# Kernel tuning notes

Hardware: AMD Instinct MI355X
Metric: run time of the kernel (lower is better)

Reference implementation:

```python
import jax, jax.numpy as jnp
import numpy as np

N_NODES = 50000
N_EDGES = 400000
D_IN = 128
D_H = 128
N_CLASSES = 20
N_GRAPHS = 256
EPS_BN = 1e-5


def _lin_params(key, d_in, d_out, scale=0.05):
    kw, kb = jax.random.split(key)
    W = jax.random.normal(kw, (d_in, d_out), jnp.float32) * scale
    b = jax.random.normal(kb, (d_out,), jnp.float32) * scale
    return W, b


def setup_inputs() -> dict:
    key = jax.random.key(0)
    ks = jax.random.split(key, 20)
    inp = {
        "x": jax.random.normal(ks[0], (N_NODES, D_IN), jnp.float32),
        "edge_index": jax.random.randint(ks[1], (2, N_EDGES), 0, N_NODES, jnp.int32),
        "batch": jnp.sort(jax.random.randint(ks[2], (N_NODES,), 0, N_GRAPHS, jnp.int32)),
    }
    kidx = 3
    for li, d_in in zip((1, 2, 3), (D_IN, D_H, D_H)):
        for nm in ("q", "k", "v", "s"):
            W, b = _lin_params(ks[kidx], d_in, D_H)
            kidx += 1
            inp[f"W{nm}{li}"] = W
            inp[f"b{nm}{li}"] = b
        inp[f"gamma{li}"] = jnp.ones((D_H,), jnp.float32)
        inp[f"beta{li}"] = jnp.zeros((D_H,), jnp.float32)
    Wl, bl = _lin_params(ks[kidx], D_H, N_CLASSES)
    inp["Wlin"] = Wl
    inp["blin"] = bl
    return inp


def _segment_softmax(logits, seg, n):
    m = jax.ops.segment_max(logits, seg, num_segments=n)
    e = jnp.exp(logits - m[seg])
    s = jax.ops.segment_sum(e, seg, num_segments=n)
    return e / (s[seg] + 1e-16)


def _transformer_conv(x, src, dst, Wq, bq, Wk, bk, Wv, bv, Ws, bs):
    # heads=1, concat=True, root_weight=True (PyG TransformerConv defaults)
    q = x @ Wq + bq  # [N, d]
    k = x @ Wk + bk
    v = x @ Wv + bv
    d = q.shape[-1]
    logits = jnp.sum(q[dst] * k[src], axis=-1) / jnp.sqrt(jnp.float32(d))  # [E]
    alpha = _segment_softmax(logits, dst, x.shape[0])
    out = jax.ops.segment_sum(alpha[:, None] * v[src], dst, num_segments=x.shape[0])
    return out + x @ Ws + bs


def _batch_norm(x, gamma, beta):
    mu = jnp.mean(x, axis=0)
    var = jnp.var(x, axis=0)
    return gamma * (x - mu) * jax.lax.rsqrt(var + EPS_BN) + beta


def _global_mean_pool(x, batch, n_graphs):
    sums = jax.ops.segment_sum(x, batch, num_segments=n_graphs)
    cnt = jax.ops.segment_sum(jnp.ones((x.shape[0],), x.dtype), batch, num_segments=n_graphs)
    return sums / jnp.maximum(cnt, 1.0)[:, None]


def reference(x, edge_index, batch,
              Wq1, bq1, Wk1, bk1, Wv1, bv1, Ws1, bs1, gamma1, beta1,
              Wq2, bq2, Wk2, bk2, Wv2, bv2, Ws2, bs2, gamma2, beta2,
              Wq3, bq3, Wk3, bk3, Wv3, bv3, Ws3, bs3, gamma3, beta3,
              Wlin, blin):
    src, dst = edge_index[0], edge_index[1]
    h = _transformer_conv(x, src, dst, Wq1, bq1, Wk1, bk1, Wv1, bv1, Ws1, bs1)
    h = jax.nn.relu(_batch_norm(h, gamma1, beta1))  # dropout inactive (eval)
    h = _transformer_conv(h, src, dst, Wq2, bq2, Wk2, bk2, Wv2, bv2, Ws2, bs2)
    h = jax.nn.relu(_batch_norm(h, gamma2, beta2))
    h = _transformer_conv(h, src, dst, Wq3, bq3, Wk3, bk3, Wv3, bv3, Ws3, bs3)
    h = jax.nn.relu(_batch_norm(h, gamma3, beta3))
    g = _global_mean_pool(h, batch, N_GRAPHS)  # [G, d]
    return g @ Wlin + blin  # [G, num_classes]
```

## Files before the change

### kernel.cpp

```cpp
#include <hip/hip_runtime.h>

#define N_NODES 50000
#define N_EDGES 400000
#define DH 128
#define N_GRAPHS 256

#define SCAN_CHUNK 512
#define N_CHUNKS ((N_NODES + SCAN_CHUNK - 1) / SCAN_CHUNK)
#define ATTN_BLOCKS ((N_NODES + 15) / 16)
#define POOL_CHUNKS ((N_NODES + 63) / 64)
#define PSLOTS 16
#define SORT_CAP 28

typedef __bf16 bf16x8 __attribute__((ext_vector_type(8)));
typedef float f32x4 __attribute__((ext_vector_type(4)));
typedef _Float16 f16x2 __attribute__((ext_vector_type(2)));
typedef _Float16 f16x8 __attribute__((ext_vector_type(8)));

#define DEV __device__ __forceinline__

#if defined(__has_builtin)
#if __has_builtin(__builtin_amdgcn_fdot2)
#define HAS_FDOT2 1
#endif
#endif

DEV float fdot2acc(f16x2 a, f16x2 b, float c) {
#ifdef HAS_FDOT2
  return __builtin_amdgcn_fdot2(a, b, c, false);
#else
  return (float)a.x * (float)b.x + (float)a.y * (float)b.y + c;
#endif
}

DEV unsigned short f2bf(float f) {
  union { float f; unsigned int i; } v; v.f = f;
  unsigned int x = v.i;
  unsigned int r = (x + 0x7fffu + ((x >> 16) & 1u)) >> 16;
  return (unsigned short)r;
}

struct WPtrs { const float* w[12]; };

__global__ void repack_kernel(WPtrs wp, unsigned short* __restrict__ WB) {
  int mat = blockIdx.y;
  int m = blockIdx.x * 256 + threadIdx.x;
  int j = m & 7;
  int lane = (m >> 3) & 63;
  int ct = (m >> 9) & 7;
  int kk = m >> 12;
  int i = kk * 32 + (lane >> 4) * 8 + j;
  int o = ct * 16 + (lane & 15);
  WB[mat * 16384 + m] = f2bf(wp.w[mat][i * 128 + o]);
}

__global__ void deg_count(const int* __restrict__ ei, int* __restrict__ deg, int E) {
  int e = blockIdx.x * 256 + threadIdx.x;
  if (e < E) atomicAdd(&deg[ei[E + e]], 1);
}

__global__ __launch_bounds__(256) void scan_sum(const int* __restrict__ deg,
                                                int* __restrict__ partials, int N) {
  __shared__ int red[256];
  int b = blockIdx.x, t = threadIdx.x;
  int base = b * SCAN_CHUNK + t * 2;
  int s = 0;
  if (base + 1 < N) { int2 v = *reinterpret_cast<const int2*>(deg + base); s = v.x + v.y; }
  else if (base < N) s = deg[base];
  red[t] = s;
  __syncthreads();
  for (int off = 128; off; off >>= 1) {
    if (t < off) red[t] += red[t + off];
    __syncthreads();
  }
  if (t == 0) partials[b] = red[0];
}

__global__ __launch_bounds__(128) void scan_partials(int* __restrict__ partials) {
  __shared__ int s[128];
  int t = threadIdx.x;
  int v = (t < N_CHUNKS) ? partials[t] : 0;
  s[t] = v;
  __syncthreads();
  for (int off = 1; off < 128; off <<= 1) {
    int o = (t >= off) ? s[t - off] : 0;
    __syncthreads();
    s[t] += o;
    __syncthreads();
  }
  if (t < N_CHUNKS) partials[t] = s[t] - v;
}

__global__ __launch_bounds__(256) void scan_apply(const int* __restrict__ deg,
                                                  const int* __restrict__ partials,
                                                  int* __restrict__ rowptr,
                                                  int* __restrict__ cursor, int N, int E) {
  __shared__ int s[256];
  int b = blockIdx.x, t = threadIdx.x;
  int base = b * SCAN_CHUNK + t * 2;
  int d0 = 0, d1 = 0;
  if (base + 1 < N) { int2 v = *reinterpret_cast<const int2*>(deg + base); d0 = v.x; d1 = v.y; }
  else if (base < N) d0 = deg[base];
  int local = d0 + d1;
  s[t] = local;
  __syncthreads();
  for (int off = 1; off < 256; off <<= 1) {
    int o = (t >= off) ? s[t - off] : 0;
    __syncthreads();
    s[t] += o;
    __syncthreads();
  }
  int offp = partials[b] + s[t] - local;
  if (base < N)     { rowptr[base] = offp;          cursor[base] = offp; }
  if (base + 1 < N) { rowptr[base + 1] = offp + d0; cursor[base + 1] = offp + d0; }
  if (b == 0 && t == 0) rowptr[N] = E;
}

__global__ void csr_scatter(const int* __restrict__ ei, int* __restrict__ cursor,
                            int* __restrict__ adj, int E) {
  int e = blockIdx.x * 256 + threadIdx.x;
  if (e < E) {
    int dst = ei[E + e];
    int pos = atomicAdd(&cursor[dst], 1);
    adj[pos] = ei[e];
  }
}

__global__ __launch_bounds__(256) void adj_sort(const int* __restrict__ rowptr,
                                                int* __restrict__ adj, int N) {
  __shared__ int buf[SORT_CAP * 256];
  int t = threadIdx.x;
  int n = blockIdx.x * 256 + t;
  if (n >= N) return;
  int p0 = rowptr[n], p1 = rowptr[n + 1];
  int d = p1 - p0;
  if (d <= 1) return;
  if (d <= SORT_CAP) {
    for (int i = 0; i < d; ++i) buf[i * 256 + t] = adj[p0 + i];
    for (int i = 1; i < d; ++i) {
      int v = buf[i * 256 + t];
      int j = i - 1;
      while (j >= 0 && buf[j * 256 + t] > v) { buf[(j + 1) * 256 + t] = buf[j * 256 + t]; --j; }
      buf[(j + 1) * 256 + t] = v;
    }
    for (int i = 0; i < d; ++i) adj[p0 + i] = buf[i * 256 + t];
  } else {
    for (int i = p0 + 1; i < p1; ++i) {
      int v = adj[i];
      int j = i - 1;
      while (j >= p0 && adj[j] > v) { adj[j + 1] = adj[j]; --j; }
      adj[j + 1] = v;
    }
  }
}

struct GemmOut { _Float16* Y[4]; const float* bias[4]; };

#define LDP 136

__global__ __launch_bounds__(256) void gemm_proj(
    const float* __restrict__ Xf,
    const _Float16* __restrict__ Hin,
    const float* __restrict__ scale, const float* __restrict__ shift,
    const unsigned short* __restrict__ WB4,
    GemmOut go, int useBN, int N)
{
  __shared__ __align__(16) unsigned short xs[64 * LDP];

  const int t = threadIdx.x;
  const int rowBase = blockIdx.x * 64;
  const int igc = (t & 15) * 8;

  if (useBN) {
    float4 sc0 = *reinterpret_cast<const float4*>(scale + igc);
    float4 sc1 = *reinterpret_cast<const float4*>(scale + igc + 4);
    float4 sh0 = *reinterpret_cast<const float4*>(shift + igc);
    float4 sh1 = *reinterpret_cast<const float4*>(shift + igc + 4);
#pragma unroll
    for (int j = 0; j < 4; ++j) {
      int v = t + 256 * j;
      int r = v >> 4;
      int grow = rowBase + r;
      ushort4 o0 = make_ushort4(0, 0, 0, 0), o1 = make_ushort4(0, 0, 0, 0);
      if (grow < N) {
        f16x8 hv = *reinterpret_cast<const f16x8*>(Hin + (size_t)grow * 128 + igc);
        o0.x = f2bf(fmaxf((float)hv[0] * sc0.x + sh0.x, 0.f));
        o0.y = f2bf(fmaxf((float)hv[1] * sc0.y + sh0.y, 0.f));
        o0.z = f2bf(fmaxf((float)hv[2] * sc0.z + sh0.z, 0.f));
        o0.w = f2bf(fmaxf((float)hv[3] * sc0.w + sh0.w, 0.f));
        o1.x = f2bf(fmaxf((float)hv[4] * sc1.x + sh1.x, 0.f));
        o1.y = f2bf(fmaxf((float)hv[5] * sc1.y + sh1.y, 0.f));
        o1.z = f2bf(fmaxf((float)hv[6] * sc1.z + sh1.z, 0.f));
        o1.w = f2bf(fmaxf((float)hv[7] * sc1.w + sh1.w, 0.f));
      }
      *reinterpret_cast<ushort4*>(&xs[r * LDP + igc]) = o0;
      *reinterpret_cast<ushort4*>(&xs[r * LDP + igc + 4]) = o1;
    }
  } else {
#pragma unroll
    for (int j = 0; j < 4; ++j) {
      int v = t + 256 * j;
      int r = v >> 4;
      int grow = rowBase + r;
      ushort4 o0 = make_ushort4(0, 0, 0, 0), o1 = make_ushort4(0, 0, 0, 0);
      if (grow < N) {
        float4 a = *reinterpret_cast<const float4*>(Xf + (size_t)grow * 128 + igc);
        float4 b = *reinterpret_cast<const float4*>(Xf + (size_t)grow * 128 + igc + 4);
        o0.x = f2bf(a.x); o0.y = f2bf(a.y); o0.z = f2bf(a.z); o0.w = f2bf(a.w);
        o1.x = f2bf(b.x); o1.y = f2bf(b.y); o1.z = f2bf(b.z); o1.w = f2bf(b.w);
      }
      *reinterpret_cast<ushort4*>(&xs[r * LDP + igc]) = o0;
      *reinterpret_cast<ushort4*>(&xs[r * LDP + igc + 4]) = o1;
    }
  }
  __syncthreads();

  const int wave = t >> 6;
  const int lane = t & 63;
  const int ln16 = lane & 15;
  const int quad = lane >> 4;
  const int r0 = wave * 16;

  bf16x8 afrag[4];
#pragma unroll
  for (int kk = 0; kk < 4; ++kk)
    afrag[kk] = *reinterpret_cast<const bf16x8*>(&xs[(r0 + ln16) * LDP + kk * 32 + quad * 8]);

  for (int proj = 0; proj < 4; ++proj) {
    const unsigned short* __restrict__ WB = WB4 + proj * 16384;
    const float* __restrict__ bias = go.bias[proj];

    f32x4 acc[8] = {};
#pragma unroll
    for (int kk = 0; kk < 4; ++kk) {
#pragma unroll
      for (int ct = 0; ct < 8; ++ct) {
        bf16x8 b = *reinterpret_cast<const bf16x8*>(WB + ((kk * 8 + ct) * 64 + lane) * 8);
        acc[ct] = __builtin_amdgcn_mfma_f32_16x16x32_bf16(afrag[kk], b, acc[ct], 0, 0, 0);
      }
    }

    _Float16* __restrict__ Yh = go.Y[proj];
#pragma unroll
    for (int ct = 0; ct < 8; ++ct) {
      int col = ct * 16 + ln16;
      float bv = bias[col];
#pragma unroll
      for (int reg = 0; reg < 4; ++reg) {
        int grow = rowBase + r0 + quad * 4 + reg;
        if (grow < N) Yh[(size_t)grow * 128 + col] = (_Float16)(acc[ct][reg] + bv);
      }
    }
  }
}

__global__ __launch_bounds__(256) void node_attn(
    const int* __restrict__ rowptr, const int* __restrict__ adj,
    const _Float16* __restrict__ Q, const _Float16* __restrict__ K,
    const _Float16* __restrict__ V, _Float16* __restrict__ H,
    float* __restrict__ Pbuf, int N)
{
  __shared__ float lsum[16][128];
  __shared__ float lsq[16][128];
  int t = threadIdx.x;
  int w = t >> 4, lane = t & 15;
  int n = blockIdx.x * 16 + w;
  bool valid = n < N;
  int nn = valid ? n : 0;
  int p0 = 0, p1 = 0;
  if (valid) { p0 = rowptr[n]; p1 = rowptr[n + 1]; }

  f16x8 qv = *reinterpret_cast<const f16x8*>(Q + (size_t)nn * 128 + lane * 8);
  f16x2 q0 = {qv[0], qv[1]}, q1 = {qv[2], qv[3]}, q2 = {qv[4], qv[5]}, q3 = {qv[6], qv[7]};

  float m = -INFINITY, s = 0.f;
  float acc[8] = {};

  int p = p0;
  for (; p + 1 < p1; p += 2) {
    int s0 = adj[p], s1 = adj[p + 1];
    f16x8 k0 = *reinterpret_cast<const f16x8*>(K + (size_t)s0 * 128 + lane * 8);
    f16x8 k1 = *reinterpret_cast<const f16x8*>(K + (size_t)s1 * 128 + lane * 8);
    float d0 = fdot2acc(q0, (f16x2){k0[0], k0[1]},
               fdot2acc(q1, (f16x2){k0[2], k0[3]},
               fdot2acc(q2, (f16x2){k0[4], k0[5]},
               fdot2acc(q3, (f16x2){k0[6], k0[7]}, 0.f))));
    float d1 = fdot2acc(q0, (f16x2){k1[0], k1[1]},
               fdot2acc(q1, (f16x2){k1[2], k1[3]},
               fdot2acc(q2, (f16x2){k1[4], k1[5]},
               fdot2acc(q3, (f16x2){k1[6], k1[7]}, 0.f))));
#pragma unroll
    for (int off = 8; off; off >>= 1) {
      d0 += __shfl_xor(d0, off, 16);
      d1 += __shfl_xor(d1, off, 16);
    }
    float l0 = d0 * 0.08838834764831845f;
    float l1 = d1 * 0.08838834764831845f;
    float mn = fmaxf(m, fmaxf(l0, l1));
    float sc = __expf(m - mn);
    float w0 = __expf(l0 - mn);
    float w1 = __expf(l1 - mn);
    f16x8 v0 = *reinterpret_cast<const f16x8*>(V + (size_t)s0 * 128 + lane * 8);
    f16x8 v1 = *reinterpret_cast<const f16x8*>(V + (size_t)s1 * 128 + lane * 8);
#pragma unroll
    for (int i = 0; i < 8; ++i)
      acc[i] = acc[i] * sc + w0 * (float)v0[i] + w1 * (float)v1[i];
    s = s * sc + w0 + w1;
    m = mn;
  }
  if (p < p1) {
    int s0 = adj[p];
    f16x8 k0 = *reinterpret_cast<const f16x8*>(K + (size_t)s0 * 128 + lane * 8);
    float d0 = fdot2acc(q0, (f16x2){k0[0], k0[1]},
               fdot2acc(q1, (f16x2){k0[2], k0[3]},
               fdot2acc(q2, (f16x2){k0[4], k0[5]},
               fdot2acc(q3, (f16x2){k0[6], k0[7]}, 0.f))));
#pragma unroll
    for (int off = 8; off; off >>= 1) d0 += __shfl_xor(d0, off, 16);
    float l0 = d0 * 0.08838834764831845f;
    float mn = fmaxf(m, l0);
    float sc = __expf(m - mn);
    float w0 = __expf(l0 - mn);
    f16x8 v0 = *reinterpret_cast<const f16x8*>(V + (size_t)s0 * 128 + lane * 8);
#pragma unroll
    for (int i = 0; i < 8; ++i)
      acc[i] = acc[i] * sc + w0 * (float)v0[i];
    s = s * sc + w0;
    m = mn;
  }

  float h[8];
#pragma unroll
  for (int i = 0; i < 8; ++i) h[i] = 0.f;
  if (valid) {
    float inv = 1.0f / (s + 1e-16f);
    f16x8 hh = *reinterpret_cast<const f16x8*>(H + (size_t)n * 128 + lane * 8);
    f16x8 ho;
#pragma unroll
    for (int i = 0; i < 8; ++i) {
      h[i] = (float)hh[i] + acc[i] * inv;
      ho[i] = (_Float16)h[i];
    }
    *reinterpret_cast<f16x8*>(H + (size_t)n * 128 + lane * 8) = ho;
  }

#pragma unroll
  for (int i = 0; i < 8; i += 4) {
    float4 hv = make_float4(h[i], h[i + 1], h[i + 2], h[i + 3]);
    float4 h2 = make_float4(hv.x * hv.x, hv.y * hv.y, hv.z * hv.z, hv.w * hv.w);
    *reinterpret_cast<float4*>(&lsum[w][lane * 8 + i]) = hv;
    *reinterpret_cast<float4*>(&lsq[w][lane * 8 + i]) = h2;
  }
  __syncthreads();

  int f = t & 127;
  float a = 0.f;
  if (t < 128) {
#pragma unroll
    for (int n16 = 0; n16 < 16; ++n16) a += lsum[n16][f];
  } else {
#pragma unroll
    for (int n16 = 0; n16 < 16; ++n16) a += lsq[n16][f];
  }
  Pbuf[(size_t)blockIdx.x * 256 + t] = a;
}

__global__ __launch_bounds__(256) void bn_reduceA(const float* __restrict__ Pbuf,
                                                  float* __restrict__ partial) {
  int t = threadIdx.x;
  float s0 = 0.f, s1 = 0.f, s2 = 0.f, s3 = 0.f;
  int r = blockIdx.x;
  for (; r + 192 < ATTN_BLOCKS; r += 256) {
    s0 += Pbuf[(size_t)(r      ) * 256 + t];
    s1 += Pbuf[(size_t)(r +  64) * 256 + t];
    s2 += Pbuf[(size_t)(r + 128) * 256 + t];
    s3 += Pbuf[(size_t)(r + 192) * 256 + t];
  }
  for (; r < ATTN_BLOCKS; r += 64) s0 += Pbuf[(size_t)r * 256 + t];
  partial[blockIdx.x * 256 + t] = s0 + s1 + s2 + s3;
}

__global__ __launch_bounds__(256) void bn_reduceB(
    const float* __restrict__ partial,
    const float* __restrict__ gamma, const float* __restrict__ beta,
    float* __restrict__ scale, float* __restrict__ shift, int N)
{
  __shared__ float red[256];
  int t = threadIdx.x;
  float s0 = 0.f, s1 = 0.f, s2 = 0.f, s3 = 0.f;
#pragma unroll
  for (int r = 0; r < 64; r += 4) {
    s0 += partial[(r + 0) * 256 + t];
    s1 += partial[(r + 1) * 256 + t];
    s2 += partial[(r + 2) * 256 + t];
    s3 += partial[(r + 3) * 256 + t];
  }
  red[t] = s0 + s1 + s2 + s3;
  __syncthreads();
  if (t < 128) {
    float mean = red[t] / (float)N;
    float var = red[t + 128] / (float)N - mean * mean;
    var = fmaxf(var, 0.f);
    float sc = gamma[t] * rsqrtf(var + 1e-5f);
    scale[t] = sc;
    shift[t] = beta[t] - mean * sc;
  }
}

__global__ __launch_bounds__(256) void pool_partial(
    const _Float16* __restrict__ H, const float* __restrict__ scale,
    const float* __restrict__ shift, const int* __restrict__ batch,
    float* __restrict__ partial, int N)
{
  int f = threadIdx.x & 127, parity = threadIdx.x >> 7;
  int base = blockIdx.x * 64;
  int lim = min(base + 64, N);
  float sc = scale[f], sh = shift[f];
  int slot = ((blockIdx.x & 7) << 1) | parity;
  int curg = -1; float s = 0.f;
  for (int row = base + parity; row < lim; row += 2) {
    int g = batch[row];
    if (g != curg) {
      if (curg >= 0) partial[(size_t)((curg << 4) | slot) * 128 + f] = s;
      curg = g; s = 0.f;
    }
    s += fmaxf((float)H[(size_t)row * 128 + f] * sc + sh, 0.f);
  }
  if (curg >= 0) partial[(size_t)((curg << 4) | slot) * 128 + f] = s;
}

__global__ __launch_bounds__(128) void final_linear(
    const float* __restrict__ partial, const int* __restrict__ batch,
    const float* __restrict__ Wlin, const float* __restrict__ blin,
    float* __restrict__ out, int N)
{
  __shared__ float pf[128];
  int g = blockIdx.x;
  int t = threadIdx.x;
  float s = 0.f;
#pragma unroll
  for (int sl = 0; sl < PSLOTS; ++sl)
    s += partial[(size_t)((g << 4) | sl) * 128 + t];
  pf[t] = s;
  __syncthreads();
  int lo = 0, hi = N;
  while (lo < hi) { int mid = (lo + hi) >> 1; if (batch[mid] < g) lo = mid + 1; else hi = mid; }
  int start = lo;
  hi = N;
  while (lo < hi) { int mid = (lo + hi) >> 1; if (batch[mid] < g + 1) lo = mid + 1; else hi = mid; }
  float inv = 1.0f / fmaxf((float)(lo - start), 1.f);
  if (t < 20) {
    float acc = 0.f;
#pragma unroll 4
    for (int i = 0; i < 128; ++i)
      acc += pf[i] * Wlin[i * 20 + t];
    out[g * 20 + t] = acc * inv + blin[t];
  }
}

extern "C" void kernel_launch(void* const* d_in, const int* in_sizes, int n_in,
                              void* d_out, int out_size, void* d_ws, size_t ws_size,
                              hipStream_t stream)
{
  const int N = N_NODES, E = N_EDGES, G = N_GRAPHS;

  const float* x = (const float*)d_in[0];
  const int* ei = (const int*)d_in[1];
  const int* batch = (const int*)d_in[2];
  const float* Wlin = (const float*)d_in[33];
  const float* blin = (const float*)d_in[34];

  char* ws = (char*)d_ws;
  size_t off = 0;
  auto alloc = [&](size_t bytes) -> void* {
    void* p = ws + off;
    off = (off + bytes + 255) & ~(size_t)255;
    return p;
  };
  unsigned short* WB = (unsigned short*)alloc(12 * 16384 * sizeof(unsigned short));
  _Float16* Qh  = (_Float16*)alloc((size_t)N * 128 * 2);
  _Float16* Kh  = (_Float16*)alloc((size_t)N * 128 * 2);
  _Float16* Vh  = (_Float16*)alloc((size_t)N * 128 * 2);
  _Float16* Hh  = (_Float16*)alloc((size_t)N * 128 * 2);
  int* deg      = (int*)alloc((size_t)N * 4);
  int* rowptr   = (int*)alloc((size_t)(N + 1) * 4);
  int* cursor   = (int*)alloc((size_t)N * 4);
  int* adj      = (int*)alloc((size_t)E * 4);
  int* partials = (int*)alloc((size_t)N_CHUNKS * 4);
  float* Pbuf   = (float*)alloc((size_t)ATTN_BLOCKS * 256 * 4);
  float* bnpart = (float*)alloc((size_t)64 * 256 * 4);
  float* scale  = (float*)alloc(128 * 4);
  float* shift  = (float*)alloc(128 * 4);
  float* ppool  = (float*)alloc((size_t)G * PSLOTS * 128 * 4);

  WPtrs wp;
  for (int L = 0; L < 3; ++L) {
    wp.w[L * 4 + 0] = (const float*)d_in[3 + L * 10 + 0];
    wp.w[L * 4 + 1] = (const float*)d_in[3 + L * 10 + 2];
    wp.w[L * 4 + 2] = (const float*)d_in[3 + L * 10 + 4];
    wp.w[L * 4 + 3] = (const float*)d_in[3 + L * 10 + 6];
  }
  repack_kernel<<<dim3(64, 12), 256, 0, stream>>>(wp, WB);

  hipMemsetAsync(deg, 0, (size_t)N * 4, stream);
  hipMemsetAsync(ppool, 0, (size_t)G * PSLOTS * 128 * 4, stream);
  deg_count<<<(E + 255) / 256, 256, 0, stream>>>(ei, deg, E);
  scan_sum<<<N_CHUNKS, 256, 0, stream>>>(deg, partials, N);
  scan_partials<<<1, 128, 0, stream>>>(partials);
  scan_apply<<<N_CHUNKS, 256, 0, stream>>>(deg, partials, rowptr, cursor, N, E);
  csr_scatter<<<(E + 255) / 256, 256, 0, stream>>>(ei, cursor, adj, E);
  adj_sort<<<(N + 255) / 256, 256, 0, stream>>>(rowptr, adj, N);

  for (int L = 0; L < 3; ++L) {
    GemmOut go;
    go.Y[0] = Qh; go.Y[1] = Kh; go.Y[2] = Vh; go.Y[3] = Hh;
    go.bias[0] = (const float*)d_in[3 + L * 10 + 1];
    go.bias[1] = (const float*)d_in[3 + L * 10 + 3];
    go.bias[2] = (const float*)d_in[3 + L * 10 + 5];
    go.bias[3] = (const float*)d_in[3 + L * 10 + 7];
    gemm_proj<<<(N + 63) / 64, 256, 0, stream>>>(
        x, Hh, scale, shift, WB + L * 4 * 16384, go, (L > 0) ? 1 : 0, N);

    node_attn<<<ATTN_BLOCKS, 256, 0, stream>>>(rowptr, adj, Qh, Kh, Vh, Hh, Pbuf, N);

    bn_reduceA<<<64, 256, 0, stream>>>(Pbuf, bnpart);
    bn_reduceB<<<1, 256, 0, stream>>>(bnpart,
        (const float*)d_in[3 + L * 10 + 8],
        (const float*)d_in[3 + L * 10 + 9],
        scale, shift, N);

    if (L == 2) {
      pool_partial<<<POOL_CHUNKS, 256, 0, stream>>>(Hh, scale, shift, batch, ppool, N);
      final_linear<<<G, 128, 0, stream>>>(ppool, batch, Wlin, blin, (float*)d_out, N);
    }
  }
}
```

Measured before the change: 468.7 us.

## Interleave K/V, stage GEMM stores via LDS, fuse BN reduce, warp-sort adjacency

Several changes land together. K and V are stored interleaved in one buffer so each edge gathers both from a single row, and the GEMM epilogue now stages fp16 results in shared memory so each row is written with vectorized 16-byte stores. The two BN reduction kernels are merged into one using a last-block ticket, and the scan-partials kernel is folded into scan_apply. Adjacency sorting becomes a 16-lane rank sort and the memsets are merged into one. Rows with degree above 32 fall back to a serial sort on a single lane, and the ticket pattern depends on correct fences.

```diff
diff --git a/kernel.cpp b/kernel.cpp
--- a/kernel.cpp
+++ b/kernel.cpp
@@ -10,7 +10,6 @@
 #define ATTN_BLOCKS ((N_NODES + 15) / 16)
 #define POOL_CHUNKS ((N_NODES + 63) / 64)
 #define PSLOTS 16
-#define SORT_CAP 28
 
 typedef __bf16 bf16x8 __attribute__((ext_vector_type(8)));
 typedef float f32x4 __attribute__((ext_vector_type(4)));
@@ -76,27 +75,25 @@
   if (t == 0) partials[b] = red[0];
 }
 
-__global__ __launch_bounds__(128) void scan_partials(int* __restrict__ partials) {
-  __shared__ int s[128];
-  int t = threadIdx.x;
-  int v = (t < N_CHUNKS) ? partials[t] : 0;
-  s[t] = v;
-  __syncthreads();
-  for (int off = 1; off < 128; off <<= 1) {
-    int o = (t >= off) ? s[t - off] : 0;
-    __syncthreads();
-    s[t] += o;
-    __syncthreads();
-  }
-  if (t < N_CHUNKS) partials[t] = s[t] - v;
-}
-
 __global__ __launch_bounds__(256) void scan_apply(const int* __restrict__ deg,
                                                   const int* __restrict__ partials,
                                                   int* __restrict__ rowptr,
                                                   int* __restrict__ cursor, int N, int E) {
   __shared__ int s[256];
+  __shared__ int prefSh;
   int b = blockIdx.x, t = threadIdx.x;
+
+  s[t] = (t < b) ? partials[t] : 0;
+  __syncthreads();
+  for (int off = 128; off; off >>= 1) {
+    if (t < off) s[t] += s[t + off];
+    __syncthreads();
+  }
+  if (t == 0) prefSh = s[0];
+  __syncthreads();
+  int pref = prefSh;
+  __syncthreads();
+
   int base = b * SCAN_CHUNK + t * 2;
   int d0 = 0, d1 = 0;
   if (base + 1 < N) { int2 v = *reinterpret_cast<const int2*>(deg + base); d0 = v.x; d1 = v.y; }
@@ -110,7 +107,7 @@
     s[t] += o;
     __syncthreads();
   }
-  int offp = partials[b] + s[t] - local;
+  int offp = pref + s[t] - local;
   if (base < N)     { rowptr[base] = offp;          cursor[base] = offp; }
   if (base + 1 < N) { rowptr[base + 1] = offp + d0; cursor[base + 1] = offp + d0; }
   if (b == 0 && t == 0) rowptr[N] = E;
@@ -126,35 +123,45 @@
   }
 }
 
-__global__ __launch_bounds__(256) void adj_sort(const int* __restrict__ rowptr,
-                                                int* __restrict__ adj, int N) {
-  __shared__ int buf[SORT_CAP * 256];
+__global__ __launch_bounds__(256) void adj_sort16(const int* __restrict__ rowptr,
+                                                  int* __restrict__ adj, int N) {
+  __shared__ int buf[16 * 32];
   int t = threadIdx.x;
-  int n = blockIdx.x * 256 + t;
-  if (n >= N) return;
-  int p0 = rowptr[n], p1 = rowptr[n + 1];
-  int d = p1 - p0;
-  if (d <= 1) return;
-  if (d <= SORT_CAP) {
-    for (int i = 0; i < d; ++i) buf[i * 256 + t] = adj[p0 + i];
-    for (int i = 1; i < d; ++i) {
-      int v = buf[i * 256 + t];
-      int j = i - 1;
-      while (j >= 0 && buf[j * 256 + t] > v) { buf[(j + 1) * 256 + t] = buf[j * 256 + t]; --j; }
-      buf[(j + 1) * 256 + t] = v;
-    }
-    for (int i = 0; i < d; ++i) adj[p0 + i] = buf[i * 256 + t];
-  } else {
-    for (int i = p0 + 1; i < p1; ++i) {
-      int v = adj[i];
-      int j = i - 1;
-      while (j >= p0 && adj[j] > v) { adj[j + 1] = adj[j]; --j; }
-      adj[j + 1] = v;
-    }
-  }
-}
-
-struct GemmOut { _Float16* Y[4]; const float* bias[4]; };
+  int g = t >> 4, l = t & 15;
+  int n = blockIdx.x * 16 + g;
+  bool valid = n < N;
+  int p0 = 0, d = 0;
+  if (valid) { p0 = rowptr[n]; d = rowptr[n + 1] - p0; }
+  if (__builtin_expect(d > 32, 0)) {
+    if (l == 0) {
+      for (int i = p0 + 1; i < p0 + d; ++i) {
+        int v = adj[i]; int j = i - 1;
+        while (j >= p0 && adj[j] > v) { adj[j + 1] = adj[j]; --j; }
+        adj[j + 1] = v;
+      }
+    }
+    d = 0;
+  }
+  int a0 = (l < d) ? adj[p0 + l] : 0x7fffffff;
+  int a1 = (16 + l < d) ? adj[p0 + 16 + l] : 0x7fffffff;
+  int r0 = 0, r1 = 0;
+#pragma unroll
+  for (int i = 0; i < 16; ++i) {
+    int v0 = __shfl(a0, i, 16);
+    int v1 = __shfl(a1, i, 16);
+    r0 += (v0 < a0) || (v0 == a0 && i < l);
+    r0 += (v1 < a0);
+    r1 += (v0 <= a1);
+    r1 += (v1 < a1) || (v1 == a1 && i < l);
+  }
+  if (l < d)      buf[g * 32 + r0] = a0;
+  if (16 + l < d) buf[g * 32 + r1] = a1;
+  __syncthreads();
+  if (l < d)      adj[p0 + l]      = buf[g * 32 + l];
+  if (16 + l < d) adj[p0 + 16 + l] = buf[g * 32 + 16 + l];
+}
+
+struct GemmOut { _Float16* Y[4]; const float* bias[4]; int ldY[4]; };
 
 #define LDP 136
 
@@ -225,6 +232,7 @@
 #pragma unroll
   for (int kk = 0; kk < 4; ++kk)
     afrag[kk] = *reinterpret_cast<const bf16x8*>(&xs[(r0 + ln16) * LDP + kk * 32 + quad * 8]);
+  __syncthreads();
 
   for (int proj = 0; proj < 4; ++proj) {
     const unsigned short* __restrict__ WB = WB4 + proj * 16384;
@@ -241,24 +249,32 @@
     }
 
     _Float16* __restrict__ Yh = go.Y[proj];
+    const int ldY = go.ldY[proj];
 #pragma unroll
     for (int ct = 0; ct < 8; ++ct) {
       int col = ct * 16 + ln16;
       float bv = bias[col];
 #pragma unroll
       for (int reg = 0; reg < 4; ++reg) {
-        int grow = rowBase + r0 + quad * 4 + reg;
-        if (grow < N) Yh[(size_t)grow * 128 + col] = (_Float16)(acc[ct][reg] + bv);
+        _Float16 hv = (_Float16)(acc[ct][reg] + bv);
+        xs[(r0 + quad * 4 + reg) * LDP + col] = __builtin_bit_cast(unsigned short, hv);
       }
+    }
+#pragma unroll
+    for (int pass = 0; pass < 4; ++pass) {
+      int rl = (lane >> 4) + pass * 4;
+      int grow = rowBase + r0 + rl;
+      f16x8 v = *reinterpret_cast<const f16x8*>(&xs[(r0 + rl) * LDP + ln16 * 8]);
+      if (grow < N)
+        *reinterpret_cast<f16x8*>(&Yh[(size_t)grow * ldY + ln16 * 8]) = v;
     }
   }
 }
 
 __global__ __launch_bounds__(256) void node_attn(
     const int* __restrict__ rowptr, const int* __restrict__ adj,
-    const _Float16* __restrict__ Q, const _Float16* __restrict__ K,
-    const _Float16* __restrict__ V, _Float16* __restrict__ H,
-    float* __restrict__ Pbuf, int N)
+    const _Float16* __restrict__ Q, const _Float16* __restrict__ KV,
+    _Float16* __restrict__ H, float* __restrict__ Pbuf, int N)
 {
   __shared__ float lsum[16][128];
   __shared__ float lsq[16][128];
@@ -279,8 +295,12 @@
   int p = p0;
   for (; p + 1 < p1; p += 2) {
     int s0 = adj[p], s1 = adj[p + 1];
-    f16x8 k0 = *reinterpret_cast<const f16x8*>(K + (size_t)s0 * 128 + lane * 8);
-    f16x8 k1 = *reinterpret_cast<const f16x8*>(K + (size_t)s1 * 128 + lane * 8);
+    const _Float16* b0 = KV + (size_t)s0 * 256 + lane * 8;
+    const _Float16* b1 = KV + (size_t)s1 * 256 + lane * 8;
+    f16x8 k0 = *reinterpret_cast<const f16x8*>(b0);
+    f16x8 k1 = *reinterpret_cast<const f16x8*>(b1);
+    f16x8 v0 = *reinterpret_cast<const f16x8*>(b0 + 128);
+    f16x8 v1 = *reinterpret_cast<const f16x8*>(b1 + 128);
     float d0 = fdot2acc(q0, (f16x2){k0[0], k0[1]},
                fdot2acc(q1, (f16x2){k0[2], k0[3]},
                fdot2acc(q2, (f16x2){k0[4], k0[5]},
@@ -300,8 +320,6 @@
     float sc = __expf(m - mn);
     float w0 = __expf(l0 - mn);
     float w1 = __expf(l1 - mn);
-    f16x8 v0 = *reinterpret_cast<const f16x8*>(V + (size_t)s0 * 128 + lane * 8);
-    f16x8 v1 = *reinterpret_cast<const f16x8*>(V + (size_t)s1 * 128 + lane * 8);
 #pragma unroll
     for (int i = 0; i < 8; ++i)
       acc[i] = acc[i] * sc + w0 * (float)v0[i] + w1 * (float)v1[i];
@@ -310,7 +328,9 @@
   }
   if (p < p1) {
     int s0 = adj[p];
-    f16x8 k0 = *reinterpret_cast<const f16x8*>(K + (size_t)s0 * 128 + lane * 8);
+    const _Float16* b0 = KV + (size_t)s0 * 256 + lane * 8;
+    f16x8 k0 = *reinterpret_cast<const f16x8*>(b0);
+    f16x8 v0 = *reinterpret_cast<const f16x8*>(b0 + 128);
     float d0 = fdot2acc(q0, (f16x2){k0[0], k0[1]},
                fdot2acc(q1, (f16x2){k0[2], k0[3]},
                fdot2acc(q2, (f16x2){k0[4], k0[5]},
@@ -321,7 +341,6 @@
     float mn = fmaxf(m, l0);
     float sc = __expf(m - mn);
     float w0 = __expf(l0 - mn);
-    f16x8 v0 = *reinterpret_cast<const f16x8*>(V + (size_t)s0 * 128 + lane * 8);
 #pragma unroll
     for (int i = 0; i < 8; ++i)
       acc[i] = acc[i] * sc + w0 * (float)v0[i];
@@ -365,35 +384,40 @@
   Pbuf[(size_t)blockIdx.x * 256 + t] = a;
 }
 
-__global__ __launch_bounds__(256) void bn_reduceA(const float* __restrict__ Pbuf,
-                                                  float* __restrict__ partial) {
-  int t = threadIdx.x;
-  float s0 = 0.f, s1 = 0.f, s2 = 0.f, s3 = 0.f;
-  int r = blockIdx.x;
-  for (; r + 192 < ATTN_BLOCKS; r += 256) {
-    s0 += Pbuf[(size_t)(r      ) * 256 + t];
-    s1 += Pbuf[(size_t)(r +  64) * 256 + t];
-    s2 += Pbuf[(size_t)(r + 128) * 256 + t];
-    s3 += Pbuf[(size_t)(r + 192) * 256 + t];
-  }
-  for (; r < ATTN_BLOCKS; r += 64) s0 += Pbuf[(size_t)r * 256 + t];
-  partial[blockIdx.x * 256 + t] = s0 + s1 + s2 + s3;
-}
-
-__global__ __launch_bounds__(256) void bn_reduceB(
-    const float* __restrict__ partial,
+__global__ __launch_bounds__(256) void bn_fused(
+    const float* __restrict__ Pbuf, float* __restrict__ bnpart,
     const float* __restrict__ gamma, const float* __restrict__ beta,
-    float* __restrict__ scale, float* __restrict__ shift, int N)
+    float* __restrict__ scale, float* __restrict__ shift,
+    int* __restrict__ ticket, int N)
 {
   __shared__ float red[256];
+  __shared__ int amLast;
   int t = threadIdx.x;
+  {
+    float s0 = 0.f, s1 = 0.f, s2 = 0.f, s3 = 0.f;
+    int r = blockIdx.x;
+    for (; r + 192 < ATTN_BLOCKS; r += 256) {
+      s0 += Pbuf[(size_t)(r      ) * 256 + t];
+      s1 += Pbuf[(size_t)(r +  64) * 256 + t];
+      s2 += Pbuf[(size_t)(r + 128) * 256 + t];
+      s3 += Pbuf[(size_t)(r + 192) * 256 + t];
+    }
+    for (; r < ATTN_BLOCKS; r += 64) s0 += Pbuf[(size_t)r * 256 + t];
+    bnpart[blockIdx.x * 256 + t] = s0 + s1 + s2 + s3;
+  }
+  __threadfence();
+  if (t == 0) amLast = (atomicAdd(ticket, 1) == 63);
+  __syncthreads();
+  if (!amLast) return;
+  __threadfence();
+
   float s0 = 0.f, s1 = 0.f, s2 = 0.f, s3 = 0.f;
 #pragma unroll
   for (int r = 0; r < 64; r += 4) {
-    s0 += partial[(r + 0) * 256 + t];
-    s1 += partial[(r + 1) * 256 + t];
-    s2 += partial[(r + 2) * 256 + t];
-    s3 += partial[(r + 3) * 256 + t];
+    s0 += bnpart[(r + 0) * 256 + t];
+    s1 += bnpart[(r + 1) * 256 + t];
+    s2 += bnpart[(r + 2) * 256 + t];
+    s3 += bnpart[(r + 3) * 256 + t];
   }
   red[t] = s0 + s1 + s2 + s3;
   __syncthreads();
@@ -479,10 +503,8 @@
   };
   unsigned short* WB = (unsigned short*)alloc(12 * 16384 * sizeof(unsigned short));
   _Float16* Qh  = (_Float16*)alloc((size_t)N * 128 * 2);
-  _Float16* Kh  = (_Float16*)alloc((size_t)N * 128 * 2);
-  _Float16* Vh  = (_Float16*)alloc((size_t)N * 128 * 2);
+  _Float16* KVh = (_Float16*)alloc((size_t)N * 256 * 2);
   _Float16* Hh  = (_Float16*)alloc((size_t)N * 128 * 2);
-  int* deg      = (int*)alloc((size_t)N * 4);
   int* rowptr   = (int*)alloc((size_t)(N + 1) * 4);
   int* cursor   = (int*)alloc((size_t)N * 4);
   int* adj      = (int*)alloc((size_t)E * 4);
@@ -491,7 +513,11 @@
   float* bnpart = (float*)alloc((size_t)64 * 256 * 4);
   float* scale  = (float*)alloc(128 * 4);
   float* shift  = (float*)alloc(128 * 4);
+  size_t zoff = off;
+  int* deg      = (int*)alloc((size_t)N * 4);
+  int* tickets  = (int*)alloc(256);
   float* ppool  = (float*)alloc((size_t)G * PSLOTS * 128 * 4);
+  size_t zbytes = off - zoff;
 
   WPtrs wp;
   for (int L = 0; L < 3; ++L) {
@@ -502,18 +528,19 @@
   }
   repack_kernel<<<dim3(64, 12), 256, 0, stream>>>(wp, WB);
 
-  hipMemsetAsync(deg, 0, (size_t)N * 4, stream);
-  hipMemsetAsync(ppool, 0, (size_t)G * PSLOTS * 128 * 4, stream);
+  hipMemsetAsync(deg, 0, zbytes, stream);
   deg_count<<<(E + 255) / 256, 256, 0, stream>>>(ei, deg, E);
   scan_sum<<<N_CHUNKS, 256, 0, stream>>>(deg, partials, N);
-  scan_partials<<<1, 128, 0, stream>>>(partials);
   scan_apply<<<N_CHUNKS, 256, 0, stream>>>(deg, partials, rowptr, cursor, N, E);
   csr_scatter<<<(E + 255) / 256, 256, 0, stream>>>(ei, cursor, adj, E);
-  adj_sort<<<(N + 255) / 256, 256, 0, stream>>>(rowptr, adj, N);
+  adj_sort16<<<ATTN_BLOCKS, 256, 0, stream>>>(rowptr, adj, N);
 
   for (int L = 0; L < 3; ++L) {
     GemmOut go;
-    go.Y[0] = Qh; go.Y[1] = Kh; go.Y[2] = Vh; go.Y[3] = Hh;
+    go.Y[0] = Qh;        go.ldY[0] = 128;
+    go.Y[1] = KVh;       go.ldY[1] = 256;
+    go.Y[2] = KVh + 128; go.ldY[2] = 256;
+    go.Y[3] = Hh;        go.ldY[3] = 128;
     go.bias[0] = (const float*)d_in[3 + L * 10 + 1];
     go.bias[1] = (const float*)d_in[3 + L * 10 + 3];
     go.bias[2] = (const float*)d_in[3 + L * 10 + 5];
@@ -521,13 +548,12 @@
     gemm_proj<<<(N + 63) / 64, 256, 0, stream>>>(
         x, Hh, scale, shift, WB + L * 4 * 16384, go, (L > 0) ? 1 : 0, N);
 
-    node_attn<<<ATTN_BLOCKS, 256, 0, stream>>>(rowptr, adj, Qh, Kh, Vh, Hh, Pbuf, N);
-
-    bn_reduceA<<<64, 256, 0, stream>>>(Pbuf, bnpart);
-    bn_reduceB<<<1, 256, 0, stream>>>(bnpart,
+    node_attn<<<ATTN_BLOCKS, 256, 0, stream>>>(rowptr, adj, Qh, KVh, Hh, Pbuf, N);
+
+    bn_fused<<<64, 256, 0, stream>>>(Pbuf, bnpart,
         (const float*)d_in[3 + L * 10 + 8],
         (const float*)d_in[3 + L * 10 + 9],
-        scale, shift, N);
+        scale, shift, tickets + L, N);
 
     if (L == 2) {
       pool_partial<<<POOL_CHUNKS, 256, 0, stream>>>(Hh, scale, shift, batch, ppool, N);
```

Measured after the change: 429.6 us. -8.3%, faster.
